# Kernel optimization log

Hardware: AMD Instinct MI355X
Metric: run time of the kernel (lower is better)

Reference implementation:

```python
import jax, jax.numpy as jnp
import numpy as np

B, D = 8192, 128          # batch, input_dim (one graph node per feature)
ENC1, ENC2 = 256, 128     # encoder hidden dims (encoder_l = 3)
DEC1, DEC2 = 64, 32       # GCN decoder feature dims (decoder_l = 2)
THRESH = 0.1              # adjacency threshold after iter > 50


def setup_inputs():
    key = jax.random.key(0)
    ks = jax.random.split(key, 10)
    f32 = jnp.float32

    def w(k, shape, scale=0.05):
        return jax.random.normal(k, shape, f32) * scale

    return {
        "x": jax.random.normal(ks[0], (B, D), f32),
        "eps": jax.random.normal(ks[1], (B, D), f32),
        "W_enc1": w(ks[2], (D, ENC1)), "b_enc1": jnp.zeros((ENC1,), f32),
        "W_enc2": w(ks[3], (ENC1, ENC2)), "b_enc2": jnp.zeros((ENC2,), f32),
        "W_mu": w(ks[4], (ENC2, D)), "b_mu": jnp.zeros((D,), f32),
        "W_lv": w(ks[5], (ENC2, D)), "b_lv": jnp.zeros((D,), f32),
        "graph_logits": jax.random.normal(ks[6], (D, D), f32),
        "W_feat": w(ks[7], (1, DEC1), 0.1),
        "W_g1": w(ks[8], (DEC1, DEC2)), "b_g1": jnp.zeros((DEC2,), f32),
        "W_g2": w(ks[9], (DEC2, 1)), "b_g2": jnp.zeros((1,), f32),
        "it": 100,
    }


def _learned_graph(graph_logits, it):
    g = jax.nn.sigmoid(graph_logits)
    eye = jnp.eye(g.shape[0], dtype=g.dtype)
    g = g * (1.0 - eye) + eye                 # force self-loops to weight 1
    if it > 50:                               # static python int -> plain if
        g = jnp.where(g < THRESH, jnp.zeros_like(g), g)
    return g


def _gcn(adj, h, W, b):
    # DGL GraphConv norm='both' with edge weights on a batch of identical
    # D-node graphs (block-diagonal batching done densely per-sample):
    #   h' = D_in^{-1/2} (A_w)^T D_out^{-1/2} h W + b
    mask = (adj > 0).astype(h.dtype)
    d_out = jnp.maximum(mask.sum(axis=1), 1.0)
    d_in = jnp.maximum(mask.sum(axis=0), 1.0)
    a_hat = adj * jax.lax.rsqrt(d_out)[:, None] * jax.lax.rsqrt(d_in)[None, :]
    msg = jnp.einsum("ij,bif->bjf", a_hat, h)  # aggregate src->dst over all batch graphs
    return msg @ W + b


def reference(x, eps, W_enc1, b_enc1, W_enc2, b_enc2, W_mu, b_mu, W_lv, b_lv,
              graph_logits, W_feat, W_g1, b_g1, W_g2, b_g2, it):
    # --- VAE encoder + reparameterize ---
    h = jax.nn.relu(x @ W_enc1 + b_enc1)
    h = jax.nn.relu(h @ W_enc2 + b_enc2)
    mu_z = h @ W_mu + b_mu
    logvar_z = h @ W_lv + b_lv
    z = mu_z + eps * jnp.exp(0.5 * logvar_z)   # (B, D)
    # --- learned adjacency over features ---
    adj = _learned_graph(graph_logits, it)     # (D, D)
    # --- graph input processor: each feature -> one node, embed its scalar ---
    hn = z[:, :, None] * W_feat[0]             # (B, D, DEC1)
    # --- homogeneous GCN decoder ---
    hn = jnp.tanh(_gcn(adj, hn, W_g1, b_g1))   # (B, D, DEC2)
    hn = _gcn(adj, hn, W_g2, b_g2)             # (B, D, 1)
    x_hat = hn.reshape(x.shape[0], -1)         # (B, D)
    return (x_hat, adj, mu_z, logvar_z)
```

## Files before the change

kernel.cpp:

```cpp
#include <hip/hip_runtime.h>
#include <math.h>

#define BATCH 8192
#define DIM   128
#define E1    256
#define E2    128
#define BRF   32

#define OUT_XHAT 0
#define OUT_ADJ  (BATCH*DIM)
#define OUT_MU   (OUT_ADJ + DIM*DIM)
#define OUT_LV   (OUT_MU + BATCH*DIM)

#define W1F   0u
#define W2F   65536u
#define WMUF  131072u
#define WLVF  163840u
#define AHF   196608u
#define COEF  229376u
#define VBUF  229408u

typedef __attribute__((ext_vector_type(8))) short s8v;
typedef __attribute__((ext_vector_type(4))) float f4v;
#define MFMA(a, b, c) __builtin_amdgcn_mfma_f32_16x16x32_bf16(a, b, c, 0, 0, 0)

__device__ __forceinline__ ushort f2bf(float f) {
    uint u = __float_as_uint(f);
    u += 0x7fffu + ((u >> 16) & 1u);
    return (ushort)(u >> 16);
}

__global__ __launch_bounds__(512) void prep_kernel(
    const float* __restrict__ W1,  const float* __restrict__ W2,
    const float* __restrict__ Wmu, const float* __restrict__ Wlv,
    const float* __restrict__ logits, const float* __restrict__ Wf,
    const float* __restrict__ Wg1, const float* __restrict__ bg1,
    const float* __restrict__ Wg2, const int* __restrict__ itp,
    float* __restrict__ out, char* __restrict__ wsb)
{
    __shared__ float gsm[16384];
    __shared__ float aux[768];
    __shared__ float vsh[32];
    const int t = threadIdx.x;

    if (blockIdx.x < 24) {
        const int tid = (int)blockIdx.x * 512 + t;
        const float* W; ushort* dst; int e, N_, ksLog;
        if (tid < 4096)       { W = W1;  dst = (ushort*)(wsb + W1F);  e = tid * 8;           N_ = 256; ksLog = 2; }
        else if (tid < 8192)  { W = W2;  dst = (ushort*)(wsb + W2F);  e = (tid - 4096) * 8;  N_ = 128; ksLog = 3; }
        else if (tid < 10240) { W = Wmu; dst = (ushort*)(wsb + WMUF); e = (tid - 8192) * 8;  N_ = 128; ksLog = 2; }
        else                  { W = Wlv; dst = (ushort*)(wsb + WLVF); e = (tid - 10240) * 8; N_ = 128; ksLog = 2; }
        const int frag = e >> 9, l = (e >> 3) & 63;
        const int nt = frag >> ksLog, ks = frag & ((1 << ksLog) - 1);
        const int k0 = ks * 32 + ((l >> 4) << 3);
        const int n  = (nt << 4) + (l & 15);
        uint pk[4];
        #pragma unroll
        for (int jj = 0; jj < 4; ++jj) {
            ushort lo = f2bf(W[(k0 + 2 * jj) * N_ + n]);
            ushort hi = f2bf(W[(k0 + 2 * jj + 1) * N_ + n]);
            pk[jj] = (uint)lo | ((uint)hi << 16);
        }
        *(uint4*)(dst + e) = make_uint4(pk[0], pk[1], pk[2], pk[3]);
        return;
    }

    const int it = itp[0];
    {
        const int j = t & 127, rq = t >> 7;
        float dp = 0.0f;
        for (int i = rq * 32; i < rq * 32 + 32; ++i) {
            float l = logits[i * DIM + j];
            float gv = 1.0f / (1.0f + expf(-l));
            if (i == j) gv = 1.0f;
            if (it > 50 && gv < 0.1f) gv = 0.0f;
            gsm[i * DIM + j] = gv;
            if (gv > 0.0f) dp += 1.0f;
        }
        aux[rq * 128 + j] = dp;
    }
    __syncthreads();
    if (t < 128) {
        float d = aux[t] + aux[128 + t] + aux[256 + t] + aux[384 + t];
        aux[512 + t] = 1.0f / sqrtf(fmaxf(d, 1.0f));
    }
    __syncthreads();
    {
        const int i = t & 127, cq = t >> 7;
        float dp = 0.0f;
        for (int c = cq * 32; c < cq * 32 + 32; ++c)
            if (gsm[i * DIM + c] > 0.0f) dp += 1.0f;
        aux[cq * 128 + i] = dp;
    }
    __syncthreads();
    if (t < 128) {
        float d = aux[t] + aux[128 + t] + aux[256 + t] + aux[384 + t];
        aux[640 + t] = 1.0f / sqrtf(fmaxf(d, 1.0f));
    }
    __syncthreads();
    for (int p = 0; p < 32; ++p) {
        int idx = t + 512 * p;
        int i = idx >> 7, j = idx & 127;
        float gv = gsm[idx];
        out[OUT_ADJ + idx] = gv;
        gsm[idx] = gv * aux[640 + i] * aux[512 + j];
    }
    if (t < 32) {
        float acc = 0.0f;
        for (int k = 0; k < 64; ++k) acc = fmaf(Wf[k], Wg1[k * 32 + t], acc);
        vsh[t] = acc;
        float* vb = (float*)(wsb + VBUF);
        vb[t] = acc; vb[32 + t] = bg1[t]; vb[64 + t] = Wg2[t];
    }
    __syncthreads();
    {
        ushort* ahf = (ushort*)(wsb + AHF);
        #pragma unroll
        for (int c = 0; c < 4; ++c) {
            int e = (t + c * 512) * 8;
            int frag = e >> 9, l = (e >> 3) & 63;
            int nt = frag >> 2, ks = frag & 3;
            int k0 = ks * 32 + ((l >> 4) << 3);
            int n  = (nt << 4) + (l & 15);
            uint pk[4];
            #pragma unroll
            for (int jj = 0; jj < 4; ++jj) {
                ushort lo = f2bf(gsm[(k0 + 2 * jj) * DIM + n]);
                ushort hi = f2bf(gsm[(k0 + 2 * jj + 1) * DIM + n]);
                pk[jj] = (uint)lo | ((uint)hi << 16);
            }
            *(uint4*)(ahf + e) = make_uint4(pk[0], pk[1], pk[2], pk[3]);
        }
    }
    if (t == 0) {
        float a1 = 0, a3 = 0, a5 = 0, vmax = 0, bmax = 0;
        for (int c = 0; c < 32; ++c) {
            float v = vsh[c], w = Wg2[c], v2 = v * v;
            a1 += w * v;
            a3 -= w * v * v2 * (1.0f / 3.0f);
            a5 += w * v * v2 * v2 * (2.0f / 15.0f);
            vmax = fmaxf(vmax, fabsf(v));
            bmax = fmaxf(bmax, fabsf(bg1[c]));
        }
        float* cf = (float*)(wsb + COEF);
        cf[0] = a1; cf[1] = a3; cf[2] = a5;
        cf[3] = (bmax == 0.0f) ? 0.2f / fmaxf(vmax, 1e-30f) : -1.0f;
    }
}

__global__ __launch_bounds__(512, 1) void fused_kernel(
    const float* __restrict__ x,   const float* __restrict__ eps,
    const float* __restrict__ b1,  const float* __restrict__ b2,
    const float* __restrict__ bmu, const float* __restrict__ blv,
    const float* __restrict__ bg2p,
    float* __restrict__ out, char* __restrict__ wsb)
{
    __shared__ __attribute__((aligned(16))) ushort bufA[4096];
    __shared__ __attribute__((aligned(16))) ushort bufB[8192];
    __shared__ __attribute__((aligned(16))) ushort bufC[4096];
    __shared__ float vls[96];

    const int t = threadIdx.x;
    const int lane = t & 63, wid = t >> 6;
    const int fr = lane & 15, fq = lane >> 4;
    const int row0 = (int)blockIdx.x * BRF;

    float epr[2][4];
    {
        const float* eb = eps + (size_t)(row0 + fq * 4) * DIM + wid * 16 + fr;
        #pragma unroll
        for (int mt = 0; mt < 2; ++mt)
            #pragma unroll
            for (int q = 0; q < 4; ++q)
                epr[mt][q] = eb[(mt * 16 + q) * DIM];
    }

    if (t < 96) vls[t] = ((const float*)(wsb + VBUF))[t];

    {
        const int r = t & 31, g = (t >> 5) & 3, ks = t >> 7;
        const float* src = x + (size_t)(row0 + r) * DIM + ks * 32 + g * 8;
        float4 u0 = *(const float4*)src;
        float4 u1 = *(const float4*)(src + 4);
        uint p0 = (uint)f2bf(u0.x) | ((uint)f2bf(u0.y) << 16);
        uint p1 = (uint)f2bf(u0.z) | ((uint)f2bf(u0.w) << 16);
        uint p2 = (uint)f2bf(u1.x) | ((uint)f2bf(u1.y) << 16);
        uint p3 = (uint)f2bf(u1.z) | ((uint)f2bf(u1.w) << 16);
        *(uint4*)&bufA[(((r >> 4) * 4 + ks) * 64 + g * 16 + (r & 15)) * 8] =
            make_uint4(p0, p1, p2, p3);
    }
    __syncthreads();

    {
        const ushort* w1f = (const ushort*)(wsb + W1F);
        f4v acc[2][2] = {{{0,0,0,0},{0,0,0,0}},{{0,0,0,0},{0,0,0,0}}};
        #pragma unroll
        for (int ks = 0; ks < 4; ++ks) {
            s8v a0 = *(const s8v*)&bufA[((0 * 4 + ks) * 64 + lane) * 8];
            s8v a1 = *(const s8v*)&bufA[((1 * 4 + ks) * 64 + lane) * 8];
            #pragma unroll
            for (int n = 0; n < 2; ++n) {
                s8v b = *(const s8v*)&w1f[(((2 * wid + n) * 4 + ks) * 64 + lane) * 8];
                acc[0][n] = MFMA(a0, b, acc[0][n]);
                acc[1][n] = MFMA(a1, b, acc[1][n]);
            }
        }
        #pragma unroll
        for (int n = 0; n < 2; ++n) {
            int col = (2 * wid + n) * 16 + fr;
            float bb = b1[col];
            #pragma unroll
            for (int mt = 0; mt < 2; ++mt) {
                int base = ((mt * 8 + (col >> 5)) * 64 + ((col >> 3) & 3) * 16) * 8 + (col & 7);
                #pragma unroll
                for (int q = 0; q < 4; ++q)
                    bufB[base + (fq * 4 + q) * 8] = f2bf(fmaxf(acc[mt][n][q] + bb, 0.0f));
            }
        }
    }
    __syncthreads();

    {
        const ushort* w2f = (const ushort*)(wsb + W2F);
        f4v acc[2] = {{0,0,0,0},{0,0,0,0}};
        #pragma unroll
        for (int ks = 0; ks < 8; ++ks) {
            s8v a0 = *(const s8v*)&bufB[((0 * 8 + ks) * 64 + lane) * 8];
            s8v a1 = *(const s8v*)&bufB[((1 * 8 + ks) * 64 + lane) * 8];
            s8v b  = *(const s8v*)&w2f[((wid * 8 + ks) * 64 + lane) * 8];
            acc[0] = MFMA(a0, b, acc[0]);
            acc[1] = MFMA(a1, b, acc[1]);
        }
        int col = wid * 16 + fr;
        float bb = b2[col];
        #pragma unroll
        for (int mt = 0; mt < 2; ++mt) {
            int base = ((mt * 4 + (col >> 5)) * 64 + ((col >> 3) & 3) * 16) * 8 + (col & 7);
            #pragma unroll
            for (int q = 0; q < 4; ++q)
                bufC[base + (fq * 4 + q) * 8] = f2bf(fmaxf(acc[mt][q] + bb, 0.0f));
        }
    }
    __syncthreads();

    {
        const ushort* wmf = (const ushort*)(wsb + WMUF);
        const ushort* wlf = (const ushort*)(wsb + WLVF);
        f4v am[2] = {{0,0,0,0},{0,0,0,0}}, al[2] = {{0,0,0,0},{0,0,0,0}};
        #pragma unroll
        for (int ks = 0; ks < 4; ++ks) {
            s8v a0 = *(const s8v*)&bufC[((0 * 4 + ks) * 64 + lane) * 8];
            s8v a1 = *(const s8v*)&bufC[((1 * 4 + ks) * 64 + lane) * 8];
            int fi = ((wid * 4 + ks) * 64 + lane) * 8;
            s8v bm = *(const s8v*)&wmf[fi];
            s8v bl = *(const s8v*)&wlf[fi];
            am[0] = MFMA(a0, bm, am[0]);
            am[1] = MFMA(a1, bm, am[1]);
            al[0] = MFMA(a0, bl, al[0]);
            al[1] = MFMA(a1, bl, al[1]);
        }
        int col = wid * 16 + fr;
        float bm = bmu[col], bl = blv[col];
        #pragma unroll
        for (int mt = 0; mt < 2; ++mt) {
            int base = ((mt * 4 + (col >> 5)) * 64 + ((col >> 3) & 3) * 16) * 8 + (col & 7);
            #pragma unroll
            for (int q = 0; q < 4; ++q) {
                int grow = row0 + mt * 16 + fq * 4 + q;
                float mu = am[mt][q] + bm;
                float lv = al[mt][q] + bl;
                out[OUT_MU + grow * DIM + col] = mu;
                out[OUT_LV + grow * DIM + col] = lv;
                float z = fmaf(epr[mt][q], __expf(0.5f * lv), mu);
                bufA[base + (fq * 4 + q) * 8] = f2bf(z);
            }
        }
    }
    __syncthreads();

    const ushort* ahf = (const ushort*)(wsb + AHF);
    const float* cf = (const float*)(wsb + COEF);
    const float a1 = cf[0], a3 = cf[1], a5 = cf[2], ssafe = cf[3];

    s8v bfr[4];
    #pragma unroll
    for (int ks = 0; ks < 4; ++ks)
        bfr[ks] = *(const s8v*)&ahf[((wid * 4 + ks) * 64 + lane) * 8];

    f4v sa[2] = {{0,0,0,0},{0,0,0,0}};
    #pragma unroll
    for (int ks = 0; ks < 4; ++ks) {
        s8v a0 = *(const s8v*)&bufA[((0 * 4 + ks) * 64 + lane) * 8];
        s8v a1 = *(const s8v*)&bufA[((1 * 4 + ks) * 64 + lane) * 8];
        sa[0] = MFMA(a0, bfr[ks], sa[0]);
        sa[1] = MFMA(a1, bfr[ks], sa[1]);
    }
    __syncthreads();

    {
        int col = wid * 16 + fr;
        #pragma unroll
        for (int mt = 0; mt < 2; ++mt) {
            int base = ((mt * 4 + (col >> 5)) * 64 + ((col >> 3) & 3) * 16) * 8 + (col & 7);
            #pragma unroll
            for (int q = 0; q < 4; ++q) {
                float s = sa[mt][q];
                float tv;
                if (fabsf(s) < ssafe) {
                    float s2 = s * s;
                    tv = s * fmaf(s2, fmaf(s2, a5, a3), a1);
                } else {
                    tv = 0.0f;
                    for (int c = 0; c < 32; ++c)
                        tv = fmaf(vls[64 + c], tanhf(fmaf(s, vls[c], vls[32 + c])), tv);
                }
                bufB[base + (fq * 4 + q) * 8] = f2bf(tv);
            }
        }
    }
    __syncthreads();

    f4v xa[2] = {{0,0,0,0},{0,0,0,0}};
    #pragma unroll
    for (int ks = 0; ks < 4; ++ks) {
        s8v a0 = *(const s8v*)&bufB[((0 * 4 + ks) * 64 + lane) * 8];
        s8v a1 = *(const s8v*)&bufB[((1 * 4 + ks) * 64 + lane) * 8];
        xa[0] = MFMA(a0, bfr[ks], xa[0]);
        xa[1] = MFMA(a1, bfr[ks], xa[1]);
    }
    const float bg2v = bg2p[0];
    {
        int col = wid * 16 + fr;
        #pragma unroll
        for (int mt = 0; mt < 2; ++mt)
            #pragma unroll
            for (int q = 0; q < 4; ++q)
                out[OUT_XHAT + (size_t)(row0 + mt * 16 + fq * 4 + q) * DIM + col] =
                    xa[mt][q] + bg2v;
    }
}

extern "C" void kernel_launch(void* const* d_in, const int* in_sizes, int n_in,
                              void* d_out, int out_size, void* d_ws, size_t ws_size,
                              hipStream_t stream)
{
    const float* x      = (const float*)d_in[0];
    const float* eps    = (const float*)d_in[1];
    const float* W1     = (const float*)d_in[2];
    const float* b1     = (const float*)d_in[3];
    const float* W2     = (const float*)d_in[4];
    const float* b2     = (const float*)d_in[5];
    const float* Wmu    = (const float*)d_in[6];
    const float* bmu    = (const float*)d_in[7];
    const float* Wlv    = (const float*)d_in[8];
    const float* blv    = (const float*)d_in[9];
    const float* logits = (const float*)d_in[10];
    const float* Wf     = (const float*)d_in[11];
    const float* Wg1    = (const float*)d_in[12];
    const float* bg1    = (const float*)d_in[13];
    const float* Wg2    = (const float*)d_in[14];
    const float* bg2    = (const float*)d_in[15];
    const int*   itp    = (const int*)d_in[16];
    float* out = (float*)d_out;
    char* wsb  = (char*)d_ws;

    hipLaunchKernelGGL(prep_kernel, dim3(25), dim3(512), 0, stream,
                       W1, W2, Wmu, Wlv, logits, Wf, Wg1, bg1, Wg2, itp, out, wsb);
    hipLaunchKernelGGL(fused_kernel, dim3(BATCH / BRF), dim3(512), 0, stream,
                       x, eps, b1, b2, bmu, blv, bg2, out, wsb);
}
```

Baseline: 25.50 us.

## Merge prep kernel into single monolithic kernel, recomputing weights and adjacency per block

Removes the separate prep kernel and its workspace buffers. Each of the 256 blocks now converts fp32 weights to bf16 MFMA fragments straight from global memory, and recomputes the adjacency degree counts, normalized adjacency fragments and tanh polynomial coefficients itself. Block 0 also writes the adjacency output. This drops one kernel launch and the dependency between the two kernels, at the cost of redundant per-block work: strided uncoalesced weight loads, repeated sigmoid evaluation over the 128x128 logits, and an extra barrier. Launch bounds are also raised to allow two blocks per CU.

```diff
diff --git a/kernel.cpp b/kernel.cpp
--- a/kernel.cpp
+++ b/kernel.cpp
@@ -12,14 +12,6 @@
 #define OUT_MU   (OUT_ADJ + DIM*DIM)
 #define OUT_LV   (OUT_MU + BATCH*DIM)
 
-#define W1F   0u
-#define W2F   65536u
-#define WMUF  131072u
-#define WLVF  163840u
-#define AHF   196608u
-#define COEF  229376u
-#define VBUF  229408u
-
 typedef __attribute__((ext_vector_type(8))) short s8v;
 typedef __attribute__((ext_vector_type(4))) float f4v;
 #define MFMA(a, b, c) __builtin_amdgcn_mfma_f32_16x16x32_bf16(a, b, c, 0, 0, 0)
@@ -30,140 +22,51 @@
     return (ushort)(u >> 16);
 }
 
-__global__ __launch_bounds__(512) void prep_kernel(
-    const float* __restrict__ W1,  const float* __restrict__ W2,
-    const float* __restrict__ Wmu, const float* __restrict__ Wlv,
+__device__ __forceinline__ float gfast(float l, int i, int j, int it) {
+    float gv = __builtin_amdgcn_rcpf(1.0f + __expf(-l));
+    if (i == j) gv = 1.0f;
+    if (it > 50 && gv < 0.1f) gv = 0.0f;
+    return gv;
+}
+
+__device__ __forceinline__ s8v ldfrag(const float* __restrict__ W, int ld,
+                                      int k0, int col) {
+    const float* p = W + (size_t)k0 * ld + col;
+    union { uint4 u; s8v v; } r;
+    float w0 = p[0],      w1 = p[ld],     w2 = p[2 * ld], w3 = p[3 * ld];
+    float w4 = p[4 * ld], w5 = p[5 * ld], w6 = p[6 * ld], w7 = p[7 * ld];
+    r.u.x = (uint)f2bf(w0) | ((uint)f2bf(w1) << 16);
+    r.u.y = (uint)f2bf(w2) | ((uint)f2bf(w3) << 16);
+    r.u.z = (uint)f2bf(w4) | ((uint)f2bf(w5) << 16);
+    r.u.w = (uint)f2bf(w6) | ((uint)f2bf(w7) << 16);
+    return r.v;
+}
+
+__global__ __launch_bounds__(512, 2) void mono_kernel(
+    const float* __restrict__ x,   const float* __restrict__ eps,
+    const float* __restrict__ W1,  const float* __restrict__ b1,
+    const float* __restrict__ W2,  const float* __restrict__ b2,
+    const float* __restrict__ Wmu, const float* __restrict__ bmu,
+    const float* __restrict__ Wlv, const float* __restrict__ blv,
     const float* __restrict__ logits, const float* __restrict__ Wf,
     const float* __restrict__ Wg1, const float* __restrict__ bg1,
-    const float* __restrict__ Wg2, const int* __restrict__ itp,
-    float* __restrict__ out, char* __restrict__ wsb)
-{
-    __shared__ float gsm[16384];
-    __shared__ float aux[768];
-    __shared__ float vsh[32];
-    const int t = threadIdx.x;
-
-    if (blockIdx.x < 24) {
-        const int tid = (int)blockIdx.x * 512 + t;
-        const float* W; ushort* dst; int e, N_, ksLog;
-        if (tid < 4096)       { W = W1;  dst = (ushort*)(wsb + W1F);  e = tid * 8;           N_ = 256; ksLog = 2; }
-        else if (tid < 8192)  { W = W2;  dst = (ushort*)(wsb + W2F);  e = (tid - 4096) * 8;  N_ = 128; ksLog = 3; }
-        else if (tid < 10240) { W = Wmu; dst = (ushort*)(wsb + WMUF); e = (tid - 8192) * 8;  N_ = 128; ksLog = 2; }
-        else                  { W = Wlv; dst = (ushort*)(wsb + WLVF); e = (tid - 10240) * 8; N_ = 128; ksLog = 2; }
-        const int frag = e >> 9, l = (e >> 3) & 63;
-        const int nt = frag >> ksLog, ks = frag & ((1 << ksLog) - 1);
-        const int k0 = ks * 32 + ((l >> 4) << 3);
-        const int n  = (nt << 4) + (l & 15);
-        uint pk[4];
-        #pragma unroll
-        for (int jj = 0; jj < 4; ++jj) {
-            ushort lo = f2bf(W[(k0 + 2 * jj) * N_ + n]);
-            ushort hi = f2bf(W[(k0 + 2 * jj + 1) * N_ + n]);
-            pk[jj] = (uint)lo | ((uint)hi << 16);
-        }
-        *(uint4*)(dst + e) = make_uint4(pk[0], pk[1], pk[2], pk[3]);
-        return;
-    }
-
-    const int it = itp[0];
-    {
-        const int j = t & 127, rq = t >> 7;
-        float dp = 0.0f;
-        for (int i = rq * 32; i < rq * 32 + 32; ++i) {
-            float l = logits[i * DIM + j];
-            float gv = 1.0f / (1.0f + expf(-l));
-            if (i == j) gv = 1.0f;
-            if (it > 50 && gv < 0.1f) gv = 0.0f;
-            gsm[i * DIM + j] = gv;
-            if (gv > 0.0f) dp += 1.0f;
-        }
-        aux[rq * 128 + j] = dp;
-    }
-    __syncthreads();
-    if (t < 128) {
-        float d = aux[t] + aux[128 + t] + aux[256 + t] + aux[384 + t];
-        aux[512 + t] = 1.0f / sqrtf(fmaxf(d, 1.0f));
-    }
-    __syncthreads();
-    {
-        const int i = t & 127, cq = t >> 7;
-        float dp = 0.0f;
-        for (int c = cq * 32; c < cq * 32 + 32; ++c)
-            if (gsm[i * DIM + c] > 0.0f) dp += 1.0f;
-        aux[cq * 128 + i] = dp;
-    }
-    __syncthreads();
-    if (t < 128) {
-        float d = aux[t] + aux[128 + t] + aux[256 + t] + aux[384 + t];
-        aux[640 + t] = 1.0f / sqrtf(fmaxf(d, 1.0f));
-    }
-    __syncthreads();
-    for (int p = 0; p < 32; ++p) {
-        int idx = t + 512 * p;
-        int i = idx >> 7, j = idx & 127;
-        float gv = gsm[idx];
-        out[OUT_ADJ + idx] = gv;
-        gsm[idx] = gv * aux[640 + i] * aux[512 + j];
-    }
-    if (t < 32) {
-        float acc = 0.0f;
-        for (int k = 0; k < 64; ++k) acc = fmaf(Wf[k], Wg1[k * 32 + t], acc);
-        vsh[t] = acc;
-        float* vb = (float*)(wsb + VBUF);
-        vb[t] = acc; vb[32 + t] = bg1[t]; vb[64 + t] = Wg2[t];
-    }
-    __syncthreads();
-    {
-        ushort* ahf = (ushort*)(wsb + AHF);
-        #pragma unroll
-        for (int c = 0; c < 4; ++c) {
-            int e = (t + c * 512) * 8;
-            int frag = e >> 9, l = (e >> 3) & 63;
-            int nt = frag >> 2, ks = frag & 3;
-            int k0 = ks * 32 + ((l >> 4) << 3);
-            int n  = (nt << 4) + (l & 15);
-            uint pk[4];
-            #pragma unroll
-            for (int jj = 0; jj < 4; ++jj) {
-                ushort lo = f2bf(gsm[(k0 + 2 * jj) * DIM + n]);
-                ushort hi = f2bf(gsm[(k0 + 2 * jj + 1) * DIM + n]);
-                pk[jj] = (uint)lo | ((uint)hi << 16);
-            }
-            *(uint4*)(ahf + e) = make_uint4(pk[0], pk[1], pk[2], pk[3]);
-        }
-    }
-    if (t == 0) {
-        float a1 = 0, a3 = 0, a5 = 0, vmax = 0, bmax = 0;
-        for (int c = 0; c < 32; ++c) {
-            float v = vsh[c], w = Wg2[c], v2 = v * v;
-            a1 += w * v;
-            a3 -= w * v * v2 * (1.0f / 3.0f);
-            a5 += w * v * v2 * v2 * (2.0f / 15.0f);
-            vmax = fmaxf(vmax, fabsf(v));
-            bmax = fmaxf(bmax, fabsf(bg1[c]));
-        }
-        float* cf = (float*)(wsb + COEF);
-        cf[0] = a1; cf[1] = a3; cf[2] = a5;
-        cf[3] = (bmax == 0.0f) ? 0.2f / fmaxf(vmax, 1e-30f) : -1.0f;
-    }
-}
-
-__global__ __launch_bounds__(512, 1) void fused_kernel(
-    const float* __restrict__ x,   const float* __restrict__ eps,
-    const float* __restrict__ b1,  const float* __restrict__ b2,
-    const float* __restrict__ bmu, const float* __restrict__ blv,
-    const float* __restrict__ bg2p,
-    float* __restrict__ out, char* __restrict__ wsb)
+    const float* __restrict__ Wg2, const float* __restrict__ bg2p,
+    const int* __restrict__ itp,
+    float* __restrict__ out)
 {
     __shared__ __attribute__((aligned(16))) ushort bufA[4096];
     __shared__ __attribute__((aligned(16))) ushort bufB[8192];
     __shared__ __attribute__((aligned(16))) ushort bufC[4096];
-    __shared__ float vls[96];
+    __shared__ float pauxA[512], pauxB[512];
+    __shared__ float rin_s[128], rdout_s[128];
+    __shared__ float vls[96], cf_s[4];
 
     const int t = threadIdx.x;
     const int lane = t & 63, wid = t >> 6;
     const int fr = lane & 15, fq = lane >> 4;
+    const int kb = fq * 8;
     const int row0 = (int)blockIdx.x * BRF;
+    const int it = itp[0];
 
     float epr[2][4];
     {
@@ -174,8 +77,6 @@
             for (int q = 0; q < 4; ++q)
                 epr[mt][q] = eb[(mt * 16 + q) * DIM];
     }
-
-    if (t < 96) vls[t] = ((const float*)(wsb + VBUF))[t];
 
     {
         const int r = t & 31, g = (t >> 5) & 3, ks = t >> 7;
@@ -189,10 +90,62 @@
         *(uint4*)&bufA[(((r >> 4) * 4 + ks) * 64 + g * 16 + (r & 15)) * 8] =
             make_uint4(p0, p1, p2, p3);
     }
-    __syncthreads();
-
-    {
-        const ushort* w1f = (const ushort*)(wsb + W1F);
+
+    {
+        const int j = t & 127, rq = t >> 7;
+        float cnt = 0.0f;
+        for (int i = rq * 32; i < rq * 32 + 32; ++i)
+            if (gfast(logits[i * DIM + j], i, j, it) > 0.0f) cnt += 1.0f;
+        pauxA[rq * 128 + j] = cnt;
+    }
+    {
+        const int i = t & 127, cq = t >> 7;
+        float cnt = 0.0f;
+        for (int c = cq * 32; c < cq * 32 + 32; ++c)
+            if (gfast(logits[i * DIM + c], i, c, it) > 0.0f) cnt += 1.0f;
+        pauxB[cq * 128 + i] = cnt;
+    }
+    if (t < 32) {
+        float acc = 0.0f;
+        for (int k = 0; k < 64; ++k) acc = fmaf(Wf[k], Wg1[k * 32 + t], acc);
+        vls[t] = acc; vls[32 + t] = bg1[t]; vls[64 + t] = Wg2[t];
+    }
+    __syncthreads();
+
+    if (t < 128) {
+        float d = pauxA[t] + pauxA[128 + t] + pauxA[256 + t] + pauxA[384 + t];
+        rin_s[t] = 1.0f / sqrtf(fmaxf(d, 1.0f));
+    } else if (t < 256) {
+        int i = t - 128;
+        float d = pauxB[i] + pauxB[128 + i] + pauxB[256 + i] + pauxB[384 + i];
+        rdout_s[i] = 1.0f / sqrtf(fmaxf(d, 1.0f));
+    } else if (t == 256) {
+        float a1 = 0, a3 = 0, a5 = 0, vmax = 0, bmax = 0;
+        for (int c = 0; c < 32; ++c) {
+            float v = vls[c], w = vls[64 + c], v2 = v * v;
+            a1 += w * v;
+            a3 -= w * v * v2 * (1.0f / 3.0f);
+            a5 += w * v * v2 * v2 * (2.0f / 15.0f);
+            vmax = fmaxf(vmax, fabsf(v));
+            bmax = fmaxf(bmax, fabsf(vls[32 + c]));
+        }
+        cf_s[0] = a1; cf_s[1] = a3; cf_s[2] = a5;
+        cf_s[3] = (bmax == 0.0f) ? 0.2f / fmaxf(vmax, 1e-30f) : -1.0f;
+    }
+
+    if (blockIdx.x == 0) {
+        const int j = t & 127, rq = t >> 7;
+        for (int i = rq * 32; i < rq * 32 + 32; ++i) {
+            float l = logits[i * DIM + j];
+            float gv = 1.0f / (1.0f + expf(-l));
+            if (i == j) gv = 1.0f;
+            if (it > 50 && gv < 0.1f) gv = 0.0f;
+            out[OUT_ADJ + i * DIM + j] = gv;
+        }
+    }
+    __syncthreads();
+
+    {
         f4v acc[2][2] = {{{0,0,0,0},{0,0,0,0}},{{0,0,0,0},{0,0,0,0}}};
         #pragma unroll
         for (int ks = 0; ks < 4; ++ks) {
@@ -200,11 +153,12 @@
             s8v a1 = *(const s8v*)&bufA[((1 * 4 + ks) * 64 + lane) * 8];
             #pragma unroll
             for (int n = 0; n < 2; ++n) {
-                s8v b = *(const s8v*)&w1f[(((2 * wid + n) * 4 + ks) * 64 + lane) * 8];
+                s8v b = ldfrag(W1, E1, ks * 32 + kb, (2 * wid + n) * 16 + fr);
                 acc[0][n] = MFMA(a0, b, acc[0][n]);
                 acc[1][n] = MFMA(a1, b, acc[1][n]);
             }
         }
+        __syncthreads();
         #pragma unroll
         for (int n = 0; n < 2; ++n) {
             int col = (2 * wid + n) * 16 + fr;
@@ -221,13 +175,12 @@
     __syncthreads();
 
     {
-        const ushort* w2f = (const ushort*)(wsb + W2F);
         f4v acc[2] = {{0,0,0,0},{0,0,0,0}};
         #pragma unroll
         for (int ks = 0; ks < 8; ++ks) {
             s8v a0 = *(const s8v*)&bufB[((0 * 8 + ks) * 64 + lane) * 8];
             s8v a1 = *(const s8v*)&bufB[((1 * 8 + ks) * 64 + lane) * 8];
-            s8v b  = *(const s8v*)&w2f[((wid * 8 + ks) * 64 + lane) * 8];
+            s8v b  = ldfrag(W2, E2, ks * 32 + kb, wid * 16 + fr);
             acc[0] = MFMA(a0, b, acc[0]);
             acc[1] = MFMA(a1, b, acc[1]);
         }
@@ -244,16 +197,13 @@
     __syncthreads();
 
     {
-        const ushort* wmf = (const ushort*)(wsb + WMUF);
-        const ushort* wlf = (const ushort*)(wsb + WLVF);
         f4v am[2] = {{0,0,0,0},{0,0,0,0}}, al[2] = {{0,0,0,0},{0,0,0,0}};
         #pragma unroll
         for (int ks = 0; ks < 4; ++ks) {
             s8v a0 = *(const s8v*)&bufC[((0 * 4 + ks) * 64 + lane) * 8];
             s8v a1 = *(const s8v*)&bufC[((1 * 4 + ks) * 64 + lane) * 8];
-            int fi = ((wid * 4 + ks) * 64 + lane) * 8;
-            s8v bm = *(const s8v*)&wmf[fi];
-            s8v bl = *(const s8v*)&wlf[fi];
+            s8v bm = ldfrag(Wmu, DIM, ks * 32 + kb, wid * 16 + fr);
+            s8v bl = ldfrag(Wlv, DIM, ks * 32 + kb, wid * 16 + fr);
             am[0] = MFMA(a0, bm, am[0]);
             am[1] = MFMA(a1, bm, am[1]);
             al[0] = MFMA(a0, bl, al[0]);
@@ -278,14 +228,27 @@
     }
     __syncthreads();
 
-    const ushort* ahf = (const ushort*)(wsb + AHF);
-    const float* cf = (const float*)(wsb + COEF);
-    const float a1 = cf[0], a3 = cf[1], a5 = cf[2], ssafe = cf[3];
-
+    const float a1c = cf_s[0], a3c = cf_s[1], a5c = cf_s[2], ssafe = cf_s[3];
+    const int acol = wid * 16 + fr;
     s8v bfr[4];
     #pragma unroll
-    for (int ks = 0; ks < 4; ++ks)
-        bfr[ks] = *(const s8v*)&ahf[((wid * 4 + ks) * 64 + lane) * 8];
+    for (int ks = 0; ks < 4; ++ks) {
+        int k0 = ks * 32 + kb;
+        float gr[8];
+        #pragma unroll
+        for (int j = 0; j < 8; ++j) {
+            int k = k0 + j;
+            float gv = gfast(logits[k * DIM + acol], k, acol, it);
+            gr[j] = gv * rdout_s[k];
+        }
+        float rj = rin_s[acol];
+        union { uint4 u; s8v v; } r;
+        r.u.x = (uint)f2bf(gr[0] * rj) | ((uint)f2bf(gr[1] * rj) << 16);
+        r.u.y = (uint)f2bf(gr[2] * rj) | ((uint)f2bf(gr[3] * rj) << 16);
+        r.u.z = (uint)f2bf(gr[4] * rj) | ((uint)f2bf(gr[5] * rj) << 16);
+        r.u.w = (uint)f2bf(gr[6] * rj) | ((uint)f2bf(gr[7] * rj) << 16);
+        bfr[ks] = r.v;
+    }
 
     f4v sa[2] = {{0,0,0,0},{0,0,0,0}};
     #pragma unroll
@@ -298,17 +261,16 @@
     __syncthreads();
 
     {
-        int col = wid * 16 + fr;
         #pragma unroll
         for (int mt = 0; mt < 2; ++mt) {
-            int base = ((mt * 4 + (col >> 5)) * 64 + ((col >> 3) & 3) * 16) * 8 + (col & 7);
+            int base = ((mt * 4 + (acol >> 5)) * 64 + ((acol >> 3) & 3) * 16) * 8 + (acol & 7);
             #pragma unroll
             for (int q = 0; q < 4; ++q) {
                 float s = sa[mt][q];
                 float tv;
                 if (fabsf(s) < ssafe) {
                     float s2 = s * s;
-                    tv = s * fmaf(s2, fmaf(s2, a5, a3), a1);
+                    tv = s * fmaf(s2, fmaf(s2, a5c, a3c), a1c);
                 } else {
                     tv = 0.0f;
                     for (int c = 0; c < 32; ++c)
@@ -329,15 +291,12 @@
         xa[1] = MFMA(a1, bfr[ks], xa[1]);
     }
     const float bg2v = bg2p[0];
-    {
-        int col = wid * 16 + fr;
-        #pragma unroll
-        for (int mt = 0; mt < 2; ++mt)
-            #pragma unroll
-            for (int q = 0; q < 4; ++q)
-                out[OUT_XHAT + (size_t)(row0 + mt * 16 + fq * 4 + q) * DIM + col] =
-                    xa[mt][q] + bg2v;
-    }
+    #pragma unroll
+    for (int mt = 0; mt < 2; ++mt)
+        #pragma unroll
+        for (int q = 0; q < 4; ++q)
+            out[OUT_XHAT + (size_t)(row0 + mt * 16 + fq * 4 + q) * DIM + acol] =
+                xa[mt][q] + bg2v;
 }
 
 extern "C" void kernel_launch(void* const* d_in, const int* in_sizes, int n_in,
@@ -362,10 +321,8 @@
     const float* bg2    = (const float*)d_in[15];
     const int*   itp    = (const int*)d_in[16];
     float* out = (float*)d_out;
-    char* wsb  = (char*)d_ws;
-
-    hipLaunchKernelGGL(prep_kernel, dim3(25), dim3(512), 0, stream,
-                       W1, W2, Wmu, Wlv, logits, Wf, Wg1, bg1, Wg2, itp, out, wsb);
-    hipLaunchKernelGGL(fused_kernel, dim3(BATCH / BRF), dim3(512), 0, stream,
-                       x, eps, b1, b2, bmu, blv, bg2, out, wsb);
-}
+
+    hipLaunchKernelGGL(mono_kernel, dim3(BATCH / BRF), dim3(512), 0, stream,
+                       x, eps, W1, b1, W2, b2, Wmu, bmu, Wlv, blv,
+                       logits, Wf, Wg1, bg1, Wg2, bg2, itp, out);
+}
```

After: 26.53 us. 1.04x slower.
